# Kernel optimization log

Measured on AMD Instinct MI355X. Metric: run time of the kernel, lower is better.

Reference implementation:

```python
import jax, jax.numpy as jnp
import numpy as np

G = 32            # gridsize
N = G * G         # num_nodes = 1024
F_IN = 32         # input_dim
H = 256           # hidden_dim
L = 4             # n_layers
B = 64            # batch
MID = F_IN + L * H
MIN_VAL = -10000000.0
EPS_LN = 1e-5
EPS_BN = 1e-5


def _grid_edges():
    ids = np.arange(N).reshape(G, G)
    hs, hd = ids[:, :-1].ravel(), ids[:, 1:].ravel()
    vs, vd = ids[:-1, :].ravel(), ids[1:, :].ravel()
    src = np.concatenate([hs, hd, vs, vd]).astype(np.int32)
    dst = np.concatenate([hd, hs, vd, vs]).astype(np.int32)
    return jnp.asarray(src), jnp.asarray(dst)


def setup_inputs() -> dict:
    key = jax.random.key(0)
    ks = jax.random.split(key, 16)
    mask_f = jax.random.bernoulli(ks[0], 0.7, (B, N)).astype(jnp.float32)
    feats = jax.random.normal(ks[1], (B, N * F_IN), dtype=jnp.float32)
    observations = jnp.concatenate([mask_f, feats], axis=1)
    src, dst = _grid_edges()
    def lin(k, fi, fo):
        return jax.random.normal(k, (fi, fo), dtype=jnp.float32) / np.sqrt(fi)
    W0 = lin(ks[2], F_IN, H); b0 = jnp.zeros((H,), jnp.float32)
    g0 = jnp.ones((H,), jnp.float32); be0 = jnp.zeros((H,), jnp.float32)
    Ws = jax.random.normal(ks[3], (L - 1, H, H), jnp.float32) / np.sqrt(H)
    bs = jnp.zeros((L - 1, H), jnp.float32)
    gs = jnp.ones((L - 1, H), jnp.float32); bes = jnp.zeros((L - 1, H), jnp.float32)
    W1 = lin(ks[4], MID, 2 * H); b1 = jnp.zeros((2 * H,), jnp.float32)
    bn_g = jnp.ones((2 * H,), jnp.float32); bn_b = jnp.zeros((2 * H,), jnp.float32)
    bn_m = jax.random.normal(ks[5], (2 * H,), jnp.float32) * 0.1
    bn_v = jax.random.uniform(ks[6], (2 * H,), jnp.float32, 0.5, 1.5)
    W2 = lin(ks[7], 2 * H, 1); b2 = jnp.zeros((1,), jnp.float32)
    return {"observations": observations, "src": src, "dst": dst,
            "W0": W0, "b0": b0, "g0": g0, "be0": be0,
            "Ws": Ws, "bs": bs, "gs": gs, "bes": bes,
            "W1": W1, "b1": b1, "bn_g": bn_g, "bn_b": bn_b,
            "bn_m": bn_m, "bn_v": bn_v, "W2": W2, "b2": b2}


def _layer_norm(z, g, b):
    mu = z.mean(-1, keepdims=True)
    var = z.var(-1, keepdims=True)
    return (z - mu) / jnp.sqrt(var + EPS_LN) * g + b


def reference(observations, src, dst, W0, b0, g0, be0, Ws, bs, gs, bes,
              W1, b1, bn_g, bn_b, bn_m, bn_v, W2, b2):
    mask = observations[:, :N] != 0.0                      # [B,N] bool action mask
    x = observations[:, N:].reshape(B, N, F_IN)            # node features
    outs = [x]
    h = x
    for l in range(L):
        # GIN with eps=-1: (1+eps)*x_i vanishes -> mlp(sum of neighbor features)
        agg = jnp.zeros_like(h).at[:, dst, :].add(h[:, src, :])
        W, bb, g, be = ((W0, b0, g0, be0) if l == 0
                        else (Ws[l - 1], bs[l - 1], gs[l - 1], bes[l - 1]))
        h = jax.nn.relu(_layer_norm(agg @ W + bb, g, be))  # mlp ReLU; outer .relu() is idempotent
        outs.append(h)
    xc = jnp.concatenate(outs, axis=-1).reshape(B * N, MID)
    z = xc @ W1 + b1
    z = (z - bn_m) / jnp.sqrt(bn_v + EPS_BN) * bn_g + bn_b  # BatchNorm1d eval mode
    z = jax.nn.relu(z)                                       # dropout off in eval
    y = (z @ W2 + b2).reshape(B, N)
    return jnp.where(mask, y, MIN_VAL)
```

## Files before the change

kernel.cpp:

```cpp
#include <hip/hip_runtime.h>
#include <stdint.h>

#define FIN 32
#define HD 256
#define MIDK 1056
#define HF 512
#define MROWS 65536
#define OBS_STRIDE 33792

typedef float f32x2 __attribute__((ext_vector_type(2)));
typedef float f32x4 __attribute__((ext_vector_type(4)));
typedef int   i32x4 __attribute__((ext_vector_type(4)));
typedef int   i32x8 __attribute__((ext_vector_type(8)));


__device__ __forceinline__ unsigned pack4fp8(float a, float b, float c, float d) {
    int w = __builtin_amdgcn_cvt_pk_fp8_f32(a, b, 0, false);
    return (unsigned)__builtin_amdgcn_cvt_pk_fp8_f32(c, d, w, true);
}
__device__ __forceinline__ unsigned char f2fp8(float f) {
    return (unsigned char)(__builtin_amdgcn_cvt_pk_fp8_f32(f, f, 0, false) & 0xff);
}

__device__ __forceinline__ void glds16(const void* g, void* l) {
    __builtin_amdgcn_global_load_lds(
        (const __attribute__((address_space(1))) unsigned int*)g,
        (__attribute__((address_space(3))) unsigned int*)l,
        16, 0, 0);
}

#define WAITV(N) asm volatile("s_waitcnt vmcnt(" #N ")" ::: "memory")
#define WAITLGKM0() asm volatile("s_waitcnt lgkmcnt(0)" ::: "memory")
__device__ __forceinline__ void barx() {
    asm volatile("" ::: "memory");
    __builtin_amdgcn_s_barrier();
    asm volatile("" ::: "memory");
}

__device__ __forceinline__ void gather16(const float* __restrict__ src, int stride, int n,
                                         unsigned char* __restrict__ dst) {
    float f[16];
#pragma unroll
    for (int j = 0; j < 16; ++j) f[j] = src[(size_t)j * stride + n];
    uint4 o;
    o.x = pack4fp8(f[0],  f[1],  f[2],  f[3]);
    o.y = pack4fp8(f[4],  f[5],  f[6],  f[7]);
    o.z = pack4fp8(f[8],  f[9],  f[10], f[11]);
    o.w = pack4fp8(f[12], f[13], f[14], f[15]);
    *(uint4*)dst = o;
}

__global__ __launch_bounds__(256) void k_prep_w(
        const float* __restrict__ W0, const float* __restrict__ Ws,
        const float* __restrict__ W1,
        unsigned char* __restrict__ Wt0, unsigned char* __restrict__ WtL,
        unsigned char* __restrict__ WtF) {
    const int b = blockIdx.x, t = threadIdx.x;
    if (b < 2) {
        int s = b * 256 + t;
        int hh = s >> 8, n = s & 255;
        gather16(W0 + (size_t)(hh * 16) * HD, HD, n, Wt0 + (size_t)s * 16);
    } else if (b < 50) {
        int u = (b - 2) * 256 + t;
        int l = u >> 12, s = u & 4095;
        int kb = s >> 9, hh = (s >> 8) & 1, n = s & 255;
        gather16(Ws + (size_t)l * 65536 + (size_t)(kb * 32 + hh * 16) * HD, HD, n,
                 WtL + (size_t)l * 65536 + (size_t)s * 16);
    } else {
        int s = (b - 50) * 256 + t;
        int it = s >> 12, r2 = s & 4095;
        int hh = r2 >> 9, n = r2 & 511;
        int k0 = it * 128 + hh * 16;
        if (k0 < MIDK)
            gather16(W1 + (size_t)k0 * HF, HF, n, WtF + (size_t)s * 16);
        else
            *(uint4*)(WtF + (size_t)s * 16) = make_uint4(0, 0, 0, 0);
    }
}

template <int K>
__global__ __launch_bounds__(256, 4) void k_layer(
        const unsigned char* __restrict__ Hin,
        const float* __restrict__ obs,
        const unsigned char* __restrict__ Wt,
        const float* __restrict__ bias, const float* __restrict__ gamma,
        const float* __restrict__ beta, unsigned char* __restrict__ Hout) {
    constexpr int KB = K / 32;
    __shared__ __align__(16) unsigned char Agg[(K / 16) * 64 * 16];
    __shared__ float ls[64], lss[64];
    const int t = threadIdx.x;
    const int w = t >> 6, lane = t & 63, quad = lane >> 4, l15 = lane & 15;
    const int q1 = quad >> 1, q0 = quad & 1;
    const int m0 = ((blockIdx.x & 7) * 128 + (blockIdx.x >> 3)) * 64;
    const int img = m0 >> 10, node0 = m0 & 1023;
    if (t < 64) { ls[t] = 0.f; lss[t] = 0.f; }

    if constexpr (K == 256) {
        const int r = t & 63, sg = t >> 6;
        const int node = node0 + r;
        const int rr = node >> 5, cc = node & 31;
        const unsigned char* Hb = Hin + (size_t)img * 262144;
#pragma unroll
        for (int p = 0; p < 2; ++p) {
            const int seg = p * 4 + sg;
            float s[32];
#pragma unroll
            for (int i = 0; i < 32; ++i) s[i] = 0.f;
            auto addn = [&](int nn) {
                uint4 u0 = *(const uint4*)(Hb + ((size_t)(2 * seg) * 1024 + nn) * 16);
                uint4 u1 = *(const uint4*)(Hb + ((size_t)(2 * seg + 1) * 1024 + nn) * 16);
                unsigned uu[8] = {u0.x, u0.y, u0.z, u0.w, u1.x, u1.y, u1.z, u1.w};
#pragma unroll
                for (int i = 0; i < 8; ++i) {
                    f32x2 lo = __builtin_amdgcn_cvt_pk_f32_fp8(uu[i], false);
                    f32x2 hi = __builtin_amdgcn_cvt_pk_f32_fp8(uu[i], true);
                    s[4 * i + 0] += lo.x; s[4 * i + 1] += lo.y;
                    s[4 * i + 2] += hi.x; s[4 * i + 3] += hi.y;
                }
            };
            if (cc > 0)  addn(node - 1);
            if (cc < 31) addn(node + 1);
            if (rr > 0)  addn(node - 32);
            if (rr < 31) addn(node + 32);
            unsigned ow[8];
#pragma unroll
            for (int i = 0; i < 8; ++i)
                ow[i] = pack4fp8(s[4 * i], s[4 * i + 1], s[4 * i + 2], s[4 * i + 3]);
            ((uint4*)Agg)[(2 * seg) * 64 + r]     = make_uint4(ow[0], ow[1], ow[2], ow[3]);
            ((uint4*)Agg)[(2 * seg + 1) * 64 + r] = make_uint4(ow[4], ow[5], ow[6], ow[7]);
        }
    } else {
        const int r = t >> 2, seg4 = t & 3;
        const int node = node0 + r;
        const int rr = node >> 5, cc = node & 31;
        const float* fb = obs + (size_t)img * OBS_STRIDE + 1024 + seg4 * 8;
        float s[8] = {0, 0, 0, 0, 0, 0, 0, 0};
        auto addnf = [&](int nn) {
            const float4* fp = (const float4*)(fb + nn * 32);
            float4 f0 = fp[0], f1 = fp[1];
            s[0] += f0.x; s[1] += f0.y; s[2] += f0.z; s[3] += f0.w;
            s[4] += f1.x; s[5] += f1.y; s[6] += f1.z; s[7] += f1.w;
        };
        if (cc > 0)  addnf(node - 1);
        if (cc < 31) addnf(node + 1);
        if (rr > 0)  addnf(node - 32);
        if (rr < 31) addnf(node + 32);
        uint2 o;
        o.x = pack4fp8(s[0], s[1], s[2], s[3]);
        o.y = pack4fp8(s[4], s[5], s[6], s[7]);
        *(uint2*)(Agg + ((seg4 >> 1) * 64 + r) * 16 + (seg4 & 1) * 8) = o;
    }
    __syncthreads();

    f32x4 acc[4][4] = {};
    const unsigned char* bbase = Wt + ((size_t)(q1 * 256 + w * 64 + l15)) * 16 + q0 * 8;
    const unsigned char* abase = Agg + ((size_t)(q1 * 64 + l15)) * 16 + q0 * 8;

#define LOADBL(dst, kb) { const unsigned char* bp = bbase + (size_t)(kb) * 8192; \
    dst[0] = *(const long long*)(bp);        dst[1] = *(const long long*)(bp + 256); \
    dst[2] = *(const long long*)(bp + 512);  dst[3] = *(const long long*)(bp + 768); }
#define MFMAL(buf, kb) { long long af[4]; \
    _Pragma("unroll") for (int mt = 0; mt < 4; ++mt) \
        af[mt] = *(const long long*)(abase + (kb) * 2048 + mt * 256); \
    _Pragma("unroll") for (int mt = 0; mt < 4; ++mt) \
    _Pragma("unroll") for (int nt = 0; nt < 4; ++nt) \
        acc[mt][nt] = __builtin_amdgcn_mfma_f32_16x16x32_fp8_fp8(af[mt], buf[nt], acc[mt][nt], 0, 0, 0); }

    if constexpr (KB == 1) {
        long long bA[4];
        LOADBL(bA, 0);
        MFMAL(bA, 0);
    } else {
        long long bA[4], bB[4];
        LOADBL(bA, 0);
#pragma unroll
        for (int j = 0; j < KB / 2 - 1; ++j) {
            LOADBL(bB, 2 * j + 1);
            MFMAL(bA, 2 * j);
            LOADBL(bA, 2 * j + 2);
            MFMAL(bB, 2 * j + 1);
        }
        LOADBL(bB, KB - 1);
        MFMAL(bA, KB - 2);
        MFMAL(bB, KB - 1);
    }
#undef LOADBL
#undef MFMAL

#pragma unroll
    for (int mt = 0; mt < 4; ++mt) {
        float s0 = 0, s1 = 0, s2 = 0, s3 = 0, u0 = 0, u1 = 0, u2 = 0, u3 = 0;
#pragma unroll
        for (int nt = 0; nt < 4; ++nt) {
            int col = w * 64 + nt * 16 + l15;
            float bv = bias[col];
            f32x4 vv = acc[mt][nt];
            vv.x += bv; vv.y += bv; vv.z += bv; vv.w += bv;
            acc[mt][nt] = vv;
            s0 += vv.x; u0 += vv.x * vv.x;
            s1 += vv.y; u1 += vv.y * vv.y;
            s2 += vv.z; u2 += vv.z * vv.z;
            s3 += vv.w; u3 += vv.w * vv.w;
        }
#pragma unroll
        for (int msk = 1; msk < 16; msk <<= 1) {
            s0 += __shfl_xor(s0, msk); u0 += __shfl_xor(u0, msk);
            s1 += __shfl_xor(s1, msk); u1 += __shfl_xor(u1, msk);
            s2 += __shfl_xor(s2, msk); u2 += __shfl_xor(u2, msk);
            s3 += __shfl_xor(s3, msk); u3 += __shfl_xor(u3, msk);
        }
        if (l15 == 0) {
            int rl = mt * 16 + quad * 4;
            atomicAdd(&ls[rl + 0], s0); atomicAdd(&lss[rl + 0], u0);
            atomicAdd(&ls[rl + 1], s1); atomicAdd(&lss[rl + 1], u1);
            atomicAdd(&ls[rl + 2], s2); atomicAdd(&lss[rl + 2], u2);
            atomicAdd(&ls[rl + 3], s3); atomicAdd(&lss[rl + 3], u3);
        }
    }
    __syncthreads();
#pragma unroll
    for (int mt = 0; mt < 4; ++mt) {
        int rl = mt * 16 + quad * 4;
        float mu0 = ls[rl + 0] * (1.f / 256.f), mu1 = ls[rl + 1] * (1.f / 256.f);
        float mu2 = ls[rl + 2] * (1.f / 256.f), mu3 = ls[rl + 3] * (1.f / 256.f);
        float rs0 = rsqrtf(lss[rl + 0] * (1.f / 256.f) - mu0 * mu0 + 1e-5f);
        float rs1 = rsqrtf(lss[rl + 1] * (1.f / 256.f) - mu1 * mu1 + 1e-5f);
        float rs2 = rsqrtf(lss[rl + 2] * (1.f / 256.f) - mu2 * mu2 + 1e-5f);
        float rs3 = rsqrtf(lss[rl + 3] * (1.f / 256.f) - mu3 * mu3 + 1e-5f);
#pragma unroll
        for (int nt = 0; nt < 4; ++nt) {
            int col = w * 64 + nt * 16 + l15;
            float gg = gamma[col], be = beta[col];
            f32x4 vv = acc[mt][nt];
            size_t rb = ((size_t)(img * 16 + w * 4 + nt) * 1024
                         + node0 + mt * 16 + quad * 4) * 16 + l15;
            Hout[rb]      = f2fp8(fmaxf((vv.x - mu0) * rs0 * gg + be, 0.f));
            Hout[rb + 16] = f2fp8(fmaxf((vv.y - mu1) * rs1 * gg + be, 0.f));
            Hout[rb + 32] = f2fp8(fmaxf((vv.z - mu2) * rs2 * gg + be, 0.f));
            Hout[rb + 48] = f2fp8(fmaxf((vv.w - mu3) * rs3 * gg + be, 0.f));
        }
    }
}

__global__ __launch_bounds__(512) void k_final(
        const unsigned char* __restrict__ h0, const unsigned char* __restrict__ h1,
        const unsigned char* __restrict__ h2, const unsigned char* __restrict__ h3,
        const unsigned char* __restrict__ WtF,
        const float* __restrict__ b1,
        const float* __restrict__ bng, const float* __restrict__ bnb,
        const float* __restrict__ bnm, const float* __restrict__ bnv,
        const float* __restrict__ W2, const float* __restrict__ b2,
        const float* __restrict__ obs, float* __restrict__ out) {
    __shared__ __align__(16) unsigned char As[2][8 * 64 * 16];
    __shared__ __align__(16) unsigned char Bsm[2][8 * 512 * 16];
    __shared__ float yred[64];
    const int t = threadIdx.x;
    const int w = t >> 6, lane = t & 63, quad = lane >> 4, l15 = lane & 15;
    const int m0 = ((blockIdx.x & 7) * 128 + (blockIdx.x >> 3)) * 64;
    const int bimg = m0 >> 10, node0 = m0 & 1023;
    if (t < 64) yred[t] = 0.f;

    const unsigned char* hbuf[4] = {h0, h1, h2, h3};
    f32x4 acc[4][4] = {};

    auto stageA = [&](int it, unsigned char* Ab) {
        int u = it * 8 + w;
        const unsigned char* src;
        if (u >= 2 && u < 66) {
            int j = u - 2;
            src = hbuf[j >> 4] + ((size_t)(bimg * 16 + (j & 15)) * 1024 + node0) * 16;
        } else {
            src = h0 + ((size_t)(bimg * 16) * 1024 + node0) * 16;
        }
        glds16(src + (size_t)lane * 16, Ab + (size_t)w * 1024);
    };
    auto stageB = [&](int it, unsigned char* Bb) {
#pragma unroll
        for (int i = 0; i < 8; ++i)
            glds16(WtF + ((size_t)it * 4096 + i * 512 + t) * 16,
                   Bb + ((size_t)(i * 512) + (t & ~63)) * 16);
    };
    auto compute = [&](const unsigned char* Ab, const unsigned char* Bb) {
        i32x8 bf[4];
#pragma unroll
        for (int nt = 0; nt < 4; ++nt) {
            const unsigned char* bp = Bb + ((size_t)(quad * 2) * 512 + w * 64 + nt * 16 + l15) * 16;
            i32x4 lo = *(const i32x4*)bp;
            i32x4 hi = *(const i32x4*)(bp + 512 * 16);
            bf[nt] = (i32x8){lo[0], lo[1], lo[2], lo[3], hi[0], hi[1], hi[2], hi[3]};
        }
#pragma unroll
        for (int mt = 0; mt < 4; ++mt) {
            const unsigned char* ap = Ab + ((size_t)(quad * 2) * 64 + mt * 16 + l15) * 16;
            i32x4 lo = *(const i32x4*)ap;
            i32x4 hi = *(const i32x4*)(ap + 64 * 16);
            i32x8 af = (i32x8){lo[0], lo[1], lo[2], lo[3], hi[0], hi[1], hi[2], hi[3]};
            __builtin_amdgcn_s_setprio(1);
#pragma unroll
            for (int nt = 0; nt < 4; ++nt)
                acc[mt][nt] = __builtin_amdgcn_mfma_scale_f32_16x16x128_f8f6f4(
                    af, bf[nt], acc[mt][nt], 0, 0, 0, 0x7F7F7F7F, 0, 0x7F7F7F7F);
            __builtin_amdgcn_s_setprio(0);
        }
    };

    if (w < 2) {
        const float* p = obs + (size_t)bimg * OBS_STRIDE + 1024 + (size_t)(node0 + lane) * 32 + w * 16;
        float4 f0 = *(const float4*)p, f1 = *(const float4*)(p + 4);
        float4 f2 = *(const float4*)(p + 8), f3 = *(const float4*)(p + 12);
        uint4 o;
        o.x = pack4fp8(f0.x, f0.y, f0.z, f0.w);
        o.y = pack4fp8(f1.x, f1.y, f1.z, f1.w);
        o.z = pack4fp8(f2.x, f2.y, f2.z, f2.w);
        o.w = pack4fp8(f3.x, f3.y, f3.z, f3.w);
        *(uint4*)(As[0] + ((size_t)w * 64 + lane) * 16) = o;
    } else {
        stageA(0, As[0]);
    }
    stageB(0, Bsm[0]);
    stageA(1, As[1]);
    stageB(1, Bsm[1]);
    WAITV(9);
    WAITLGKM0();
    barx();
    compute(As[0], Bsm[0]);
    barx();

#pragma unroll 1
    for (int it = 1; it < 9; ++it) {
        const int cur = it & 1;
        if (it < 8) {
            stageA(it + 1, As[cur ^ 1]);
            stageB(it + 1, Bsm[cur ^ 1]);
            WAITV(9);
        } else {
            WAITV(0);
        }
        barx();
        compute(As[cur], Bsm[cur]);
        barx();
    }

    float scv[4], sbv[4], w2v[4];
#pragma unroll
    for (int nt = 0; nt < 4; ++nt) {
        int col = w * 64 + nt * 16 + l15;
        float sc = bng[col] * rsqrtf(bnv[col] + 1e-5f);
        scv[nt] = sc;
        sbv[nt] = (b1[col] - bnm[col]) * sc + bnb[col];
        w2v[nt] = W2[col];
    }
#pragma unroll
    for (int mt = 0; mt < 4; ++mt) {
        float p0 = 0, p1 = 0, p2 = 0, p3 = 0;
#pragma unroll
        for (int nt = 0; nt < 4; ++nt) {
            f32x4 vv = acc[mt][nt];
            p0 += fmaxf(vv.x * scv[nt] + sbv[nt], 0.f) * w2v[nt];
            p1 += fmaxf(vv.y * scv[nt] + sbv[nt], 0.f) * w2v[nt];
            p2 += fmaxf(vv.z * scv[nt] + sbv[nt], 0.f) * w2v[nt];
            p3 += fmaxf(vv.w * scv[nt] + sbv[nt], 0.f) * w2v[nt];
        }
#pragma unroll
        for (int msk = 1; msk < 16; msk <<= 1) {
            p0 += __shfl_xor(p0, msk);
            p1 += __shfl_xor(p1, msk);
            p2 += __shfl_xor(p2, msk);
            p3 += __shfl_xor(p3, msk);
        }
        if (l15 == 0) {
            int rl = mt * 16 + quad * 4;
            atomicAdd(&yred[rl + 0], p0);
            atomicAdd(&yred[rl + 1], p1);
            atomicAdd(&yred[rl + 2], p2);
            atomicAdd(&yred[rl + 3], p3);
        }
    }
    __syncthreads();
    if (t < 64) {
        int gm = m0 + t;
        float mk = obs[(size_t)bimg * OBS_STRIDE + (node0 + t)];
        out[gm] = (mk != 0.f) ? yred[t] + b2[0] : -10000000.0f;
    }
}

extern "C" void kernel_launch(void* const* d_in, const int* in_sizes, int n_in,
                              void* d_out, int out_size, void* d_ws, size_t ws_size,
                              hipStream_t stream) {
    const float* obs = (const float*)d_in[0];
    const float* W0  = (const float*)d_in[3];
    const float* b0  = (const float*)d_in[4];
    const float* g0  = (const float*)d_in[5];
    const float* be0 = (const float*)d_in[6];
    const float* Ws  = (const float*)d_in[7];
    const float* bs  = (const float*)d_in[8];
    const float* gs  = (const float*)d_in[9];
    const float* bes = (const float*)d_in[10];
    const float* W1  = (const float*)d_in[11];
    const float* b1  = (const float*)d_in[12];
    const float* bng = (const float*)d_in[13];
    const float* bnb = (const float*)d_in[14];
    const float* bnm = (const float*)d_in[15];
    const float* bnv = (const float*)d_in[16];
    const float* W2  = (const float*)d_in[17];
    const float* b2  = (const float*)d_in[18];
    float* out = (float*)d_out;

    char* ws = (char*)d_ws;
    unsigned char* h0  = (unsigned char*)(ws);
    unsigned char* h1  = (unsigned char*)(ws + 16777216);
    unsigned char* h2  = (unsigned char*)(ws + 33554432);
    unsigned char* h3  = (unsigned char*)(ws + 50331648);
    unsigned char* Wt0 = (unsigned char*)(ws + 67108864);
    unsigned char* WtL = (unsigned char*)(ws + 67117056);
    unsigned char* WtF = (unsigned char*)(ws + 67313664);

    k_prep_w<<<194, 256, 0, stream>>>(W0, Ws, W1, Wt0, WtL, WtF);

    k_layer<FIN><<<1024, 256, 0, stream>>>(h0 , obs, Wt0, b0, g0, be0, h0);
    k_layer<HD> <<<1024, 256, 0, stream>>>(h0, obs, WtL,              bs,       gs,       bes,       h1);
    k_layer<HD> <<<1024, 256, 0, stream>>>(h1, obs, WtL + 65536,      bs + 256, gs + 256, bes + 256, h2);
    k_layer<HD> <<<1024, 256, 0, stream>>>(h2, obs, WtL + 2 * 65536,  bs + 512, gs + 512, bes + 512, h3);

    k_final<<<1024, 512, 0, stream>>>(h0, h1, h2, h3, WtF, b1, bng, bnb, bnm, bnv,
                                      W2, b2, obs, out);
}
```

Measured before the change: 237.3 us.

## Load final-GEMM weights directly to registers and stage whole A tile upfront

In the final fused GEMM kernel, the double-buffered LDS pipeline for both A and B is removed. The full 64-row A tile (all K chunks) is loaded into LDS once with a single barrier. Each wave then reads its B (weight) fragments straight from global memory into registers, using a two-register-set software pipeline interleaved with MFMAs. This removes per-iteration barriers and the LDS round trip for the weights. In exchange it adds register pressure and relies on L2 to serve the repeated weight reads across blocks, with LDS use rising to about 72KB.

```diff
diff --git a/kernel.cpp b/kernel.cpp
--- a/kernel.cpp
+++ b/kernel.cpp
@@ -251,8 +251,7 @@
         const float* __restrict__ bnm, const float* __restrict__ bnv,
         const float* __restrict__ W2, const float* __restrict__ b2,
         const float* __restrict__ obs, float* __restrict__ out) {
-    __shared__ __align__(16) unsigned char As[2][8 * 64 * 16];
-    __shared__ __align__(16) unsigned char Bsm[2][8 * 512 * 16];
+    __shared__ __align__(16) unsigned char As[72 * 64 * 16];
     __shared__ float yred[64];
     const int t = threadIdx.x;
     const int w = t >> 6, lane = t & 63, quad = lane >> 4, l15 = lane & 15;
@@ -262,47 +261,6 @@
 
     const unsigned char* hbuf[4] = {h0, h1, h2, h3};
     f32x4 acc[4][4] = {};
-
-    auto stageA = [&](int it, unsigned char* Ab) {
-        int u = it * 8 + w;
-        const unsigned char* src;
-        if (u >= 2 && u < 66) {
-            int j = u - 2;
-            src = hbuf[j >> 4] + ((size_t)(bimg * 16 + (j & 15)) * 1024 + node0) * 16;
-        } else {
-            src = h0 + ((size_t)(bimg * 16) * 1024 + node0) * 16;
-        }
-        glds16(src + (size_t)lane * 16, Ab + (size_t)w * 1024);
-    };
-    auto stageB = [&](int it, unsigned char* Bb) {
-#pragma unroll
-        for (int i = 0; i < 8; ++i)
-            glds16(WtF + ((size_t)it * 4096 + i * 512 + t) * 16,
-                   Bb + ((size_t)(i * 512) + (t & ~63)) * 16);
-    };
-    auto compute = [&](const unsigned char* Ab, const unsigned char* Bb) {
-        i32x8 bf[4];
-#pragma unroll
-        for (int nt = 0; nt < 4; ++nt) {
-            const unsigned char* bp = Bb + ((size_t)(quad * 2) * 512 + w * 64 + nt * 16 + l15) * 16;
-            i32x4 lo = *(const i32x4*)bp;
-            i32x4 hi = *(const i32x4*)(bp + 512 * 16);
-            bf[nt] = (i32x8){lo[0], lo[1], lo[2], lo[3], hi[0], hi[1], hi[2], hi[3]};
-        }
-#pragma unroll
-        for (int mt = 0; mt < 4; ++mt) {
-            const unsigned char* ap = Ab + ((size_t)(quad * 2) * 64 + mt * 16 + l15) * 16;
-            i32x4 lo = *(const i32x4*)ap;
-            i32x4 hi = *(const i32x4*)(ap + 64 * 16);
-            i32x8 af = (i32x8){lo[0], lo[1], lo[2], lo[3], hi[0], hi[1], hi[2], hi[3]};
-            __builtin_amdgcn_s_setprio(1);
-#pragma unroll
-            for (int nt = 0; nt < 4; ++nt)
-                acc[mt][nt] = __builtin_amdgcn_mfma_scale_f32_16x16x128_f8f6f4(
-                    af, bf[nt], acc[mt][nt], 0, 0, 0, 0x7F7F7F7F, 0, 0x7F7F7F7F);
-            __builtin_amdgcn_s_setprio(0);
-        }
-    };
 
     if (w < 2) {
         const float* p = obs + (size_t)bimg * OBS_STRIDE + 1024 + (size_t)(node0 + lane) * 32 + w * 16;
@@ -313,33 +271,60 @@
         o.y = pack4fp8(f1.x, f1.y, f1.z, f1.w);
         o.z = pack4fp8(f2.x, f2.y, f2.z, f2.w);
         o.w = pack4fp8(f3.x, f3.y, f3.z, f3.w);
-        *(uint4*)(As[0] + ((size_t)w * 64 + lane) * 16) = o;
-    } else {
-        stageA(0, As[0]);
-    }
-    stageB(0, Bsm[0]);
-    stageA(1, As[1]);
-    stageB(1, Bsm[1]);
-    WAITV(9);
+        *(uint4*)(As + ((size_t)w * 64 + lane) * 16) = o;
+    }
+#pragma unroll
+    for (int j = 0; j < 9; ++j) {
+        int u = 2 + w + 8 * j;
+        if (u < 72) {
+            int jj = u - 2;
+            const unsigned char* src;
+            if (jj < 64)
+                src = hbuf[jj >> 4] + ((size_t)(bimg * 16 + (jj & 15)) * 1024 + node0) * 16;
+            else
+                src = h0 + ((size_t)(bimg * 16) * 1024 + node0) * 16;
+            glds16(src + (size_t)lane * 16, As + (size_t)u * 1024);
+        }
+    }
+    WAITV(0);
     WAITLGKM0();
     barx();
-    compute(As[0], Bsm[0]);
-    barx();
-
-#pragma unroll 1
-    for (int it = 1; it < 9; ++it) {
-        const int cur = it & 1;
-        if (it < 8) {
-            stageA(it + 1, As[cur ^ 1]);
-            stageB(it + 1, Bsm[cur ^ 1]);
-            WAITV(9);
-        } else {
-            WAITV(0);
-        }
-        barx();
-        compute(As[cur], Bsm[cur]);
-        barx();
-    }
+
+    const unsigned char* bwave = WtF + ((size_t)(quad * 2) * 512 + w * 64 + l15) * 16;
+    const unsigned char* awave = As + ((size_t)(quad * 2) * 64 + l15) * 16;
+
+#define LOADB(dst, it) { const unsigned char* bp = bwave + (size_t)(it) * 65536; \
+    _Pragma("unroll") for (int nt = 0; nt < 4; ++nt) { \
+        dst[nt][0] = *(const i32x4*)(bp + nt * 256); \
+        dst[nt][1] = *(const i32x4*)(bp + nt * 256 + 8192); } }
+#define MFMAK(buf, it) { \
+    _Pragma("unroll") for (int mt = 0; mt < 4; ++mt) { \
+        const unsigned char* ap = awave + (size_t)(it) * 8192 + mt * 256; \
+        i32x4 alo = *(const i32x4*)ap; \
+        i32x4 ahi = *(const i32x4*)(ap + 1024); \
+        i32x8 af = (i32x8){alo[0], alo[1], alo[2], alo[3], ahi[0], ahi[1], ahi[2], ahi[3]}; \
+        __builtin_amdgcn_s_setprio(1); \
+        _Pragma("unroll") for (int nt = 0; nt < 4; ++nt) { \
+            i32x8 bf = (i32x8){buf[nt][0][0], buf[nt][0][1], buf[nt][0][2], buf[nt][0][3], \
+                               buf[nt][1][0], buf[nt][1][1], buf[nt][1][2], buf[nt][1][3]}; \
+            acc[mt][nt] = __builtin_amdgcn_mfma_scale_f32_16x16x128_f8f6f4( \
+                af, bf, acc[mt][nt], 0, 0, 0, 0x7F7F7F7F, 0, 0x7F7F7F7F); } \
+        __builtin_amdgcn_s_setprio(0); } }
+
+    {
+        i32x4 Ba[4][2], Bb[4][2];
+        LOADB(Ba, 0);
+#pragma unroll
+        for (int j = 0; j < 4; ++j) {
+            LOADB(Bb, 2 * j + 1);
+            MFMAK(Ba, 2 * j);
+            LOADB(Ba, 2 * j + 2);
+            MFMAK(Bb, 2 * j + 1);
+        }
+        MFMAK(Ba, 8);
+    }
+#undef LOADB
+#undef MFMAK
 
     float scv[4], sbv[4], w2v[4];
 #pragma unroll
```

New measurement: 214.9 us, median of 3. 9.5% less time.
